# Performance work log

Measured on AMD Instinct MI355X. Metric: run time of the kernel, lower is better.

The kernel has to match this reference:

```python
import jax, jax.numpy as jnp
import numpy as np
import math

SEQ_LEN, PRED_LEN, CHANNELS, RANK = 720, 336, 862, 32
IN_LEN = SEQ_LEN // 2  # Haar low-pass with stride 2 (seq_len even)
BATCH = 256


def _dct2_ortho_mat(N):
    # D[k, n] = s_k * 2 * cos(pi * k * (2n+1) / (2N)); orthonormal DCT-II
    k = np.arange(N)[:, None]
    n = np.arange(N)[None, :]
    D = 2.0 * np.cos(np.pi * k * (2 * n + 1) / (2 * N))
    s = np.full(N, np.sqrt(1.0 / (2 * N)))
    s[0] = np.sqrt(1.0 / (4 * N))
    return jnp.asarray((s[:, None] * D).astype(np.float32))


def _idct2_unnorm_mat(N):
    # scipy.fft.idct(type=2, norm=None): out[n] = (1/N) * (x0/2 + sum_{k>=1} x_k cos(pi k (2n+1)/(2N)))
    # Returned as M[k, n] so that out = x @ M along last axis.
    k = np.arange(N)[:, None]
    n = np.arange(N)[None, :]
    M = np.cos(np.pi * k * (2 * n + 1) / (2 * N)) / N
    M[0, :] *= 0.5
    return jnp.asarray(M.astype(np.float32))


D_DCT = _dct2_ortho_mat(IN_LEN)        # [IN_LEN, IN_LEN]
M_IDCT = _idct2_unnorm_mat(PRED_LEN)   # [PRED_LEN, PRED_LEN]
INV_SQRT2 = 1.0 / math.sqrt(2.0)


def setup_inputs() -> dict:
    key = jax.random.key(0)
    k1, k2, k3, k4 = jax.random.split(key, 4)
    x = jax.random.normal(k1, (BATCH, SEQ_LEN, CHANNELS), dtype=jnp.float32)
    # kaiming_uniform-like scales for LowRank params
    boundA = math.sqrt(6.0 / IN_LEN)
    boundB = math.sqrt(6.0 / RANK)
    A = jax.random.uniform(k2, (IN_LEN, RANK), dtype=jnp.float32, minval=-boundA, maxval=boundA)
    B = jax.random.uniform(k3, (RANK, PRED_LEN), dtype=jnp.float32, minval=-boundB, maxval=boundB)
    b = jax.random.uniform(k4, (PRED_LEN,), dtype=jnp.float32)
    return {"x": x, "A": A, "B": B, "b": b}


def reference(x, A, B, b):
    # x: [B, L, C] -> [B, C, L]
    xt = jnp.transpose(x, (0, 2, 1))
    seq_mean = jnp.mean(xt, axis=-1, keepdims=True)          # [B, C, 1]
    xc = xt - seq_mean
    # Haar low-pass: depthwise conv1d with [1,1]/sqrt(2), stride 2
    h = (xc[..., ::2] + xc[..., 1::2]) * INV_SQRT2           # [B, C, IN_LEN]
    # orthonormal DCT-II along last axis, then divide by length
    y = jnp.einsum('bcn,kn->bck', h, D_DCT) / IN_LEN         # [B, C, IN_LEN]
    # low-rank prediction head (shared across channels)
    z = (y @ A) @ B + b                                      # [B, C, PRED_LEN]
    # unnormalized inverse DCT-II (scipy idct type=2, norm=None)
    o = z @ M_IDCT                                           # [B, C, PRED_LEN]
    o = o + seq_mean
    return jnp.transpose(o, (0, 2, 1))                       # [B, PRED_LEN, C]
```

## Files before the change

### kernel.cpp

```cpp
#include <hip/hip_runtime.h>
#include <math.h>

#define SEQ_LEN   720
#define IN_LEN    360
#define PRED_LEN  336
#define CHANNELS  862
#define RANK      32
#define BATCH     256

typedef _Float16 h2 __attribute__((ext_vector_type(2)));

#define WS_WH    0
#define WS_VH    5760
#define WS_CV    11136

#define L_EX     0
#define L_W      29376
#define L_V      35136
#define L_CV     40512

__device__ __forceinline__ float fdot2w(h2 a, h2 b, float c) {
#if __has_builtin(__builtin_amdgcn_fdot2)
    return __builtin_amdgcn_fdot2(a, b, c, false);
#else
    return fmaf((float)a[0], (float)b[0], fmaf((float)a[1], (float)b[1], c));
#endif
}
__device__ __forceinline__ h2 pkrtz(float a, float b) {
    return __builtin_bit_cast(h2, __builtin_amdgcn_cvt_pkrtz(a, b));
}
#define BC(u)  __builtin_bit_cast(h2, (u))
#define BCU(v) __builtin_bit_cast(unsigned, (v))

__device__ __forceinline__ void ntstore2(float* p, float2 v) {
    __builtin_nontemporal_store(__builtin_bit_cast(unsigned long long, v),
                                (unsigned long long*)p);
}

__global__ __launch_bounds__(256) void k_prep(const float* __restrict__ A,
                                              const float* __restrict__ B,
                                              const float* __restrict__ bias,
                                              unsigned* __restrict__ Wh,
                                              unsigned* __restrict__ Vh,
                                              float* __restrict__ cvec) {
    __shared__ float sbuf[IN_LEN * RANK];
    __shared__ float sres[256];
    const int t = threadIdx.x;
    int blk = blockIdx.x;
    if (blk < 45) {
        for (int i = t; i < IN_LEN * RANK; i += 256) sbuf[i] = A[i];
        __syncthreads();
        int n = blk * 8 + (t >> 5), r = t & 31;
        int step = 2 * n + 1, m = 0;
        float sum = 0.f;
        for (int k = 0; k < IN_LEN; ++k) {
            float coef = (k == 0) ? 0.05270462766947299f
                                  : 0.07453559924999299f;
            float d = coef * cospif((float)m * (1.0f / 720.0f));
            sum = fmaf(d, sbuf[k * RANK + r], sum);
            m += step; if (m >= 1440) m -= 1440;
        }
        sres[t] = sum * 0.0019641855032960957f;
        __syncthreads();
        if (t < 128) {
            int nl = t >> 4, j = t & 15;
            h2 v = pkrtz(sres[nl * 32 + 2 * j], sres[nl * 32 + 2 * j + 1]);
            Wh[(blk * 8 + nl) * 16 + j] = BCU(v);
        }
    } else if (blk < 87) {
        for (int i = t; i < PRED_LEN * RANK; i += 256) {
            int r = i / PRED_LEN, k = i - r * PRED_LEN;
            sbuf[k * RANK + r] = B[i];
        }
        __syncthreads();
        int n = (blk - 45) * 8 + (t >> 5), r = t & 31;
        int step = 2 * n + 1, m = 0;
        float sum = 0.f;
        for (int k = 0; k < PRED_LEN; ++k) {
            float mk = cospif((float)m * (1.0f / 672.0f));
            if (k == 0) mk *= 0.5f;
            sum = fmaf(mk, sbuf[k * RANK + r], sum);
            m += step; if (m >= 1344) m -= 1344;
        }
        sres[t] = sum * (1.0f / 336.0f);
        __syncthreads();
        if (t < 128) {
            int nl = t >> 4, j = t & 15;
            h2 v = pkrtz(sres[nl * 32 + 2 * j], sres[nl * 32 + 2 * j + 1]);
            Vh[((blk - 45) * 8 + nl) * 16 + j] = BCU(v);
        }
    } else {
        int n = (blk - 87) * 256 + t;
        if (n < PRED_LEN) {
            int step = 2 * n + 1, m = 0;
            float sum = 0.f;
            for (int k = 0; k < PRED_LEN; ++k) {
                float mk = cospif((float)m * (1.0f / 672.0f));
                if (k == 0) mk *= 0.5f;
                sum = fmaf(mk, bias[k], sum);
                m += step; if (m >= 1344) m -= 1344;
            }
            cvec[n] = sum * (1.0f / 336.0f);
        }
    }
}

__global__ __launch_bounds__(512) void k_main(const float* __restrict__ x,
                                              const float* __restrict__ A,
                                              const unsigned* __restrict__ Wh,
                                              const unsigned* __restrict__ Vh,
                                              const float* __restrict__ cvec,
                                              float* __restrict__ out) {
    __shared__ unsigned ldsu[40848];
    const int tid = threadIdx.x;
    const int b = blockIdx.x;
    const int h = tid >> 8;
    const int i = tid & 255;
    const bool active = (i < 216);
    const int c0 = (i < 215) ? 4 * i : 858;

    for (int idx = tid; idx < 1440; idx += 512)
        ((uint4*)(ldsu + L_W))[idx] = ((const uint4*)Wh)[idx];
    for (int idx = tid; idx < 1344; idx += 512)
        ((uint4*)(ldsu + L_V))[idx] = ((const uint4*)Vh)[idx];
    for (int idx = tid; idx < 84; idx += 512)
        ((uint4*)(ldsu + L_CV))[idx] = ((const uint4*)cvec)[idx];
    __syncthreads();

    h2 acc0[16], acc1[16], acc2[16], acc3[16];
    #pragma unroll
    for (int j = 0; j < 16; ++j) {
        acc0[j] = pkrtz(0.f, 0.f); acc1[j] = pkrtz(0.f, 0.f);
        acc2[j] = pkrtz(0.f, 0.f); acc3[j] = pkrtz(0.f, 0.f);
    }
    float S0 = 0.f, S1 = 0.f, S2 = 0.f, S3 = 0.f;

    if (active) {
        const float* xp = x + (size_t)b * (SEQ_LEN * CHANNELS)
                            + (size_t)h * (IN_LEN * CHANNELS) + c0;
        float2 b0[4], b1[4], b2[4], b3[4];
        #define LOADN(BUF, NL) { const float* p_ = xp + (size_t)(2 * (NL)) * CHANNELS; \
            BUF[0] = *(const float2*)(p_);                 \
            BUF[1] = *(const float2*)(p_ + 2);             \
            BUF[2] = *(const float2*)(p_ + CHANNELS);      \
            BUF[3] = *(const float2*)(p_ + CHANNELS + 2); }

        #define BODY(BUF, NL) { \
            float p0 = BUF[0].x + BUF[2].x; \
            float p1 = BUF[0].y + BUF[2].y; \
            float p2 = BUF[1].x + BUF[3].x; \
            float p3 = BUF[1].y + BUF[3].y; \
            S0 += p0; S1 += p1; S2 += p2; S3 += p3; \
            h2 P0 = pkrtz(p0, p0), P1 = pkrtz(p1, p1); \
            h2 P2 = pkrtz(p2, p2), P3 = pkrtz(p3, p3); \
            const uint4* wr = (const uint4*)(ldsu + L_W) + ((NL) + 180 * h) * 4; \
            _Pragma("unroll") \
            for (int q_ = 0; q_ < 4; ++q_) { \
                uint4 wv = wr[q_]; \
                h2 w0 = BC(wv.x), w1 = BC(wv.y), w2 = BC(wv.z), w3 = BC(wv.w); \
                acc0[4*q_+0] = w0 * P0 + acc0[4*q_+0]; \
                acc1[4*q_+0] = w0 * P1 + acc1[4*q_+0]; \
                acc2[4*q_+0] = w0 * P2 + acc2[4*q_+0]; \
                acc3[4*q_+0] = w0 * P3 + acc3[4*q_+0]; \
                acc0[4*q_+1] = w1 * P0 + acc0[4*q_+1]; \
                acc1[4*q_+1] = w1 * P1 + acc1[4*q_+1]; \
                acc2[4*q_+1] = w1 * P2 + acc2[4*q_+1]; \
                acc3[4*q_+1] = w1 * P3 + acc3[4*q_+1]; \
                acc0[4*q_+2] = w2 * P0 + acc0[4*q_+2]; \
                acc1[4*q_+2] = w2 * P1 + acc1[4*q_+2]; \
                acc2[4*q_+2] = w2 * P2 + acc2[4*q_+2]; \
                acc3[4*q_+2] = w2 * P3 + acc3[4*q_+2]; \
                acc0[4*q_+3] = w3 * P0 + acc0[4*q_+3]; \
                acc1[4*q_+3] = w3 * P1 + acc1[4*q_+3]; \
                acc2[4*q_+3] = w3 * P2 + acc2[4*q_+3]; \
                acc3[4*q_+3] = w3 * P3 + acc3[4*q_+3]; \
            } }

        LOADN(b0, 0) LOADN(b1, 1) LOADN(b2, 2)
        for (int it = 0; it < 45; ++it) {
            const int base = 4 * it;
            LOADN(b3, base + 3)
            BODY(b0, base)
            { int nn = (base + 4 < 180) ? base + 4 : 179; LOADN(b0, nn) }
            BODY(b1, base + 1)
            { int nn = (base + 5 < 180) ? base + 5 : 179; LOADN(b1, nn) }
            BODY(b2, base + 2)
            { int nn = (base + 6 < 180) ? base + 6 : 179; LOADN(b2, nn) }
            BODY(b3, base + 3)
        }
        #undef BODY
        #undef LOADN
    }

    if (active) {
        uint4* rec = (uint4*)(ldsu + (i + 216 * h) * 68);
        #pragma unroll
        for (int q = 0; q < 4; ++q) {
            uint4 v;
            v.x = BCU(acc0[4*q+0]); v.y = BCU(acc0[4*q+1]);
            v.z = BCU(acc0[4*q+2]); v.w = BCU(acc0[4*q+3]);
            rec[q] = v;
            v.x = BCU(acc1[4*q+0]); v.y = BCU(acc1[4*q+1]);
            v.z = BCU(acc1[4*q+2]); v.w = BCU(acc1[4*q+3]);
            rec[4 + q] = v;
            v.x = BCU(acc2[4*q+0]); v.y = BCU(acc2[4*q+1]);
            v.z = BCU(acc2[4*q+2]); v.w = BCU(acc2[4*q+3]);
            rec[8 + q] = v;
            v.x = BCU(acc3[4*q+0]); v.y = BCU(acc3[4*q+1]);
            v.z = BCU(acc3[4*q+2]); v.w = BCU(acc3[4*q+3]);
            rec[12 + q] = v;
        }
        uint4 sv;
        sv.x = __float_as_uint(S0); sv.y = __float_as_uint(S1);
        sv.z = __float_as_uint(S2); sv.w = __float_as_uint(S3);
        rec[16] = sv;
    }
    __syncthreads();

    if (active) {
        const uint4* pr = (const uint4*)(ldsu + (i + 216 * (1 - h)) * 68);
        #pragma unroll
        for (int q = 0; q < 4; ++q) {
            uint4 v = pr[q];
            acc0[4*q+0] = acc0[4*q+0] + BC(v.x); acc0[4*q+1] = acc0[4*q+1] + BC(v.y);
            acc0[4*q+2] = acc0[4*q+2] + BC(v.z); acc0[4*q+3] = acc0[4*q+3] + BC(v.w);
            v = pr[4 + q];
            acc1[4*q+0] = acc1[4*q+0] + BC(v.x); acc1[4*q+1] = acc1[4*q+1] + BC(v.y);
            acc1[4*q+2] = acc1[4*q+2] + BC(v.z); acc1[4*q+3] = acc1[4*q+3] + BC(v.w);
            v = pr[8 + q];
            acc2[4*q+0] = acc2[4*q+0] + BC(v.x); acc2[4*q+1] = acc2[4*q+1] + BC(v.y);
            acc2[4*q+2] = acc2[4*q+2] + BC(v.z); acc2[4*q+3] = acc2[4*q+3] + BC(v.w);
            v = pr[12 + q];
            acc3[4*q+0] = acc3[4*q+0] + BC(v.x); acc3[4*q+1] = acc3[4*q+1] + BC(v.y);
            acc3[4*q+2] = acc3[4*q+2] + BC(v.z); acc3[4*q+3] = acc3[4*q+3] + BC(v.w);
        }
        uint4 sv = pr[16];
        float S0f = S0 + __uint_as_float(sv.x), S1f = S1 + __uint_as_float(sv.y);
        float S2f = S2 + __uint_as_float(sv.z), S3f = S3 + __uint_as_float(sv.w);

        const float kc = (1.0f / 360.0f) * 0.037267799624996496f;
        float g0 = -S0f * kc, g1 = -S1f * kc, g2 = -S2f * kc, g3 = -S3f * kc;
        h2 G0 = pkrtz(g0, g0), G1 = pkrtz(g1, g1), G2 = pkrtz(g2, g2), G3 = pkrtz(g3, g3);
        #pragma unroll
        for (int q = 0; q < 8; ++q) {
            float4 a4 = ((const float4*)A)[q];
            h2 aa = pkrtz(a4.x, a4.y), ab = pkrtz(a4.z, a4.w);
            acc0[2*q]   = aa * G0 + acc0[2*q];   acc0[2*q+1] = ab * G0 + acc0[2*q+1];
            acc1[2*q]   = aa * G1 + acc1[2*q];   acc1[2*q+1] = ab * G1 + acc1[2*q+1];
            acc2[2*q]   = aa * G2 + acc2[2*q];   acc2[2*q+1] = ab * G2 + acc2[2*q+1];
            acc3[2*q]   = aa * G3 + acc3[2*q];   acc3[2*q+1] = ab * G3 + acc3[2*q+1];
        }
        const float mean0 = S0f * (1.0f / 720.0f), mean1 = S1f * (1.0f / 720.0f);
        const float mean2 = S2f * (1.0f / 720.0f), mean3 = S3f * (1.0f / 720.0f);

        float* op = out + (size_t)b * (PRED_LEN * CHANNELS)
                        + (size_t)(168 * h) * CHANNELS + c0;
        for (int nl = 0; nl < 168; ++nl) {
            const int n = 168 * h + nl;
            const uint4* vr = (const uint4*)(ldsu + L_V) + n * 4;
            float o0 = 0.f, o1 = 0.f, o2 = 0.f, o3 = 0.f;
            float e0 = 0.f, e1 = 0.f, e2 = 0.f, e3 = 0.f;
            #pragma unroll
            for (int q = 0; q < 4; ++q) {
                uint4 v = vr[q];
                h2 v0 = BC(v.x), v1 = BC(v.y), v2 = BC(v.z), v3 = BC(v.w);
                o0 = fdot2w(acc0[4*q+0], v0, o0); e0 = fdot2w(acc0[4*q+1], v1, e0);
                o1 = fdot2w(acc1[4*q+0], v0, o1); e1 = fdot2w(acc1[4*q+1], v1, e1);
                o2 = fdot2w(acc2[4*q+0], v0, o2); e2 = fdot2w(acc2[4*q+1], v1, e2);
                o3 = fdot2w(acc3[4*q+0], v0, o3); e3 = fdot2w(acc3[4*q+1], v1, e3);
                o0 = fdot2w(acc0[4*q+2], v2, o0); e0 = fdot2w(acc0[4*q+3], v3, e0);
                o1 = fdot2w(acc1[4*q+2], v2, o1); e1 = fdot2w(acc1[4*q+3], v3, e1);
                o2 = fdot2w(acc2[4*q+2], v2, o2); e2 = fdot2w(acc2[4*q+3], v3, e2);
                o3 = fdot2w(acc3[4*q+2], v2, o3); e3 = fdot2w(acc3[4*q+3], v3, e3);
            }
            float cvn = ((const float*)(ldsu + L_CV))[n];
            float2 w0, w1;
            w0.x = (o0 + e0) + cvn + mean0;
            w0.y = (o1 + e1) + cvn + mean1;
            w1.x = (o2 + e2) + cvn + mean2;
            w1.y = (o3 + e3) + cvn + mean3;
            ntstore2(op,     w0);
            ntstore2(op + 2, w1);
            op += CHANNELS;
        }
    }
}


extern "C" void kernel_launch(void* const* d_in, const int* in_sizes, int n_in,
                              void* d_out, int out_size, void* d_ws, size_t ws_size,
                              hipStream_t stream) {
    (void)in_sizes; (void)n_in; (void)out_size; (void)ws_size;
    const float* x    = (const float*)d_in[0];
    const float* A    = (const float*)d_in[1];
    const float* B    = (const float*)d_in[2];
    const float* bias = (const float*)d_in[3];
    float* out = (float*)d_out;

    unsigned* Wh   = (unsigned*)d_ws + WS_WH;
    unsigned* Vh   = (unsigned*)d_ws + WS_VH;
    float*    cvec = (float*)d_ws + WS_CV;

    k_prep<<<dim3(89), dim3(256), 0, stream>>>(A, B, bias, Wh, Vh, cvec);
    k_main<<<dim3(BATCH), dim3(512), 0, stream>>>(x, A, Wh, Vh, cvec, out);
}
```

Baseline: 249.0 us.

## Split channels across two blocks per batch and shrink LDS footprint

The grid becomes 2 x BATCH with 256-thread blocks, each block covering half the channels, where before one 512-thread block handled a whole batch. LDS is cut from about 160KB to about 59KB: the W matrix and the V matrix now share one region, with V loaded after the first phase. The cross-half accumulator exchange is done in two smaller rounds to fit the smaller buffer. The goal is more resident blocks per CU and better latency hiding, at the cost of extra barriers and reloading V from global memory after the reduction phase.

```diff
diff --git a/kernel.cpp b/kernel.cpp
--- a/kernel.cpp
+++ b/kernel.cpp
@@ -14,10 +14,10 @@
 #define WS_VH    5760
 #define WS_CV    11136
 
-#define L_EX     0
-#define L_W      29376
-#define L_V      35136
-#define L_CV     40512
+#define L_A      0
+#define L_EX     5760
+#define L_CV     14400
+#define L_TOT    14736
 
 __device__ __forceinline__ float fdot2w(h2 a, h2 b, float c) {
 #if __has_builtin(__builtin_amdgcn_fdot2)
@@ -32,7 +32,8 @@
 #define BC(u)  __builtin_bit_cast(h2, (u))
 #define BCU(v) __builtin_bit_cast(unsigned, (v))
 
-__device__ __forceinline__ void ntstore2(float* p, float2 v) {
+__device__ __forceinline__ void ntstore8(float* p, float a, float b) {
+    float2 v; v.x = a; v.y = b;
     __builtin_nontemporal_store(__builtin_bit_cast(unsigned long long, v),
                                 (unsigned long long*)p);
 }
@@ -105,25 +106,25 @@
     }
 }
 
-__global__ __launch_bounds__(512) void k_main(const float* __restrict__ x,
+__global__ __launch_bounds__(256) void k_main(const float* __restrict__ x,
                                               const float* __restrict__ A,
                                               const unsigned* __restrict__ Wh,
                                               const unsigned* __restrict__ Vh,
                                               const float* __restrict__ cvec,
                                               float* __restrict__ out) {
-    __shared__ unsigned ldsu[40848];
+    __shared__ unsigned ldsu[L_TOT];
     const int tid = threadIdx.x;
-    const int b = blockIdx.x;
-    const int h = tid >> 8;
-    const int i = tid & 255;
-    const bool active = (i < 216);
-    const int c0 = (i < 215) ? 4 * i : 858;
-
-    for (int idx = tid; idx < 1440; idx += 512)
-        ((uint4*)(ldsu + L_W))[idx] = ((const uint4*)Wh)[idx];
-    for (int idx = tid; idx < 1344; idx += 512)
-        ((uint4*)(ldsu + L_V))[idx] = ((const uint4*)Vh)[idx];
-    for (int idx = tid; idx < 84; idx += 512)
+    const int s = blockIdx.x;
+    const int b = blockIdx.y;
+    const int h = tid >> 7;
+    const int i = tid & 127;
+    const bool active = (i < 108);
+    int c0 = s * 432 + 4 * i;
+    if (c0 > 858) c0 = 858;
+
+    for (int idx = tid; idx < 1440; idx += 256)
+        ((uint4*)(ldsu + L_A))[idx] = ((const uint4*)Wh)[idx];
+    for (int idx = tid; idx < 84; idx += 256)
         ((uint4*)(ldsu + L_CV))[idx] = ((const uint4*)cvec)[idx];
     __syncthreads();
 
@@ -153,7 +154,7 @@
             S0 += p0; S1 += p1; S2 += p2; S3 += p3; \
             h2 P0 = pkrtz(p0, p0), P1 = pkrtz(p1, p1); \
             h2 P2 = pkrtz(p2, p2), P3 = pkrtz(p3, p3); \
-            const uint4* wr = (const uint4*)(ldsu + L_W) + ((NL) + 180 * h) * 4; \
+            const uint4* wr = (const uint4*)(ldsu + L_A) + ((NL) + 180 * h) * 4; \
             _Pragma("unroll") \
             for (int q_ = 0; q_ < 4; ++q_) { \
                 uint4 wv = wr[q_]; \
@@ -176,70 +177,87 @@
                 acc3[4*q_+3] = w3 * P3 + acc3[4*q_+3]; \
             } }
 
+        #define CL(nn) ((nn) < 180 ? (nn) : 179)
         LOADN(b0, 0) LOADN(b1, 1) LOADN(b2, 2)
         for (int it = 0; it < 45; ++it) {
             const int base = 4 * it;
-            LOADN(b3, base + 3)
-            BODY(b0, base)
-            { int nn = (base + 4 < 180) ? base + 4 : 179; LOADN(b0, nn) }
-            BODY(b1, base + 1)
-            { int nn = (base + 5 < 180) ? base + 5 : 179; LOADN(b1, nn) }
-            BODY(b2, base + 2)
-            { int nn = (base + 6 < 180) ? base + 6 : 179; LOADN(b2, nn) }
-            BODY(b3, base + 3)
-        }
+            LOADN(b3, base + 3)      BODY(b0, base)
+            LOADN(b0, CL(base + 4))  BODY(b1, base + 1)
+            LOADN(b1, CL(base + 5))  BODY(b2, base + 2)
+            LOADN(b2, CL(base + 6))  BODY(b3, base + 3)
+        }
+        #undef CL
         #undef BODY
         #undef LOADN
     }
-
-    if (active) {
-        uint4* rec = (uint4*)(ldsu + (i + 216 * h) * 68);
+    __syncthreads();
+
+    for (int idx = tid; idx < 1344; idx += 256)
+        ((uint4*)(ldsu + L_A))[idx] = ((const uint4*)Vh)[idx];
+    if (active) {
+        unsigned* rec = ldsu + L_EX + (i + 108 * h) * 40;
         #pragma unroll
         for (int q = 0; q < 4; ++q) {
             uint4 v;
             v.x = BCU(acc0[4*q+0]); v.y = BCU(acc0[4*q+1]);
             v.z = BCU(acc0[4*q+2]); v.w = BCU(acc0[4*q+3]);
-            rec[q] = v;
+            ((uint4*)rec)[q] = v;
             v.x = BCU(acc1[4*q+0]); v.y = BCU(acc1[4*q+1]);
             v.z = BCU(acc1[4*q+2]); v.w = BCU(acc1[4*q+3]);
-            rec[4 + q] = v;
+            ((uint4*)rec)[4 + q] = v;
+        }
+        rec[32] = __float_as_uint(S0);
+        rec[33] = __float_as_uint(S1);
+    }
+    __syncthreads();
+    if (active) {
+        const unsigned* pr = ldsu + L_EX + (i + 108 * (1 - h)) * 40;
+        #pragma unroll
+        for (int q = 0; q < 4; ++q) {
+            uint4 v = ((const uint4*)pr)[q];
+            acc0[4*q+0] = acc0[4*q+0] + BC(v.x); acc0[4*q+1] = acc0[4*q+1] + BC(v.y);
+            acc0[4*q+2] = acc0[4*q+2] + BC(v.z); acc0[4*q+3] = acc0[4*q+3] + BC(v.w);
+            v = ((const uint4*)pr)[4 + q];
+            acc1[4*q+0] = acc1[4*q+0] + BC(v.x); acc1[4*q+1] = acc1[4*q+1] + BC(v.y);
+            acc1[4*q+2] = acc1[4*q+2] + BC(v.z); acc1[4*q+3] = acc1[4*q+3] + BC(v.w);
+        }
+        S0 += __uint_as_float(pr[32]);
+        S1 += __uint_as_float(pr[33]);
+    }
+    __syncthreads();
+
+    if (active) {
+        unsigned* rec = ldsu + L_EX + (i + 108 * h) * 40;
+        #pragma unroll
+        for (int q = 0; q < 4; ++q) {
+            uint4 v;
             v.x = BCU(acc2[4*q+0]); v.y = BCU(acc2[4*q+1]);
             v.z = BCU(acc2[4*q+2]); v.w = BCU(acc2[4*q+3]);
-            rec[8 + q] = v;
+            ((uint4*)rec)[q] = v;
             v.x = BCU(acc3[4*q+0]); v.y = BCU(acc3[4*q+1]);
             v.z = BCU(acc3[4*q+2]); v.w = BCU(acc3[4*q+3]);
-            rec[12 + q] = v;
-        }
-        uint4 sv;
-        sv.x = __float_as_uint(S0); sv.y = __float_as_uint(S1);
-        sv.z = __float_as_uint(S2); sv.w = __float_as_uint(S3);
-        rec[16] = sv;
-    }
-    __syncthreads();
-
-    if (active) {
-        const uint4* pr = (const uint4*)(ldsu + (i + 216 * (1 - h)) * 68);
+            ((uint4*)rec)[4 + q] = v;
+        }
+        rec[32] = __float_as_uint(S2);
+        rec[33] = __float_as_uint(S3);
+    }
+    __syncthreads();
+    if (active) {
+        const unsigned* pr = ldsu + L_EX + (i + 108 * (1 - h)) * 40;
         #pragma unroll
         for (int q = 0; q < 4; ++q) {
-            uint4 v = pr[q];
-            acc0[4*q+0] = acc0[4*q+0] + BC(v.x); acc0[4*q+1] = acc0[4*q+1] + BC(v.y);
-            acc0[4*q+2] = acc0[4*q+2] + BC(v.z); acc0[4*q+3] = acc0[4*q+3] + BC(v.w);
-            v = pr[4 + q];
-            acc1[4*q+0] = acc1[4*q+0] + BC(v.x); acc1[4*q+1] = acc1[4*q+1] + BC(v.y);
-            acc1[4*q+2] = acc1[4*q+2] + BC(v.z); acc1[4*q+3] = acc1[4*q+3] + BC(v.w);
-            v = pr[8 + q];
+            uint4 v = ((const uint4*)pr)[q];
             acc2[4*q+0] = acc2[4*q+0] + BC(v.x); acc2[4*q+1] = acc2[4*q+1] + BC(v.y);
             acc2[4*q+2] = acc2[4*q+2] + BC(v.z); acc2[4*q+3] = acc2[4*q+3] + BC(v.w);
-            v = pr[12 + q];
+            v = ((const uint4*)pr)[4 + q];
             acc3[4*q+0] = acc3[4*q+0] + BC(v.x); acc3[4*q+1] = acc3[4*q+1] + BC(v.y);
             acc3[4*q+2] = acc3[4*q+2] + BC(v.z); acc3[4*q+3] = acc3[4*q+3] + BC(v.w);
         }
-        uint4 sv = pr[16];
-        float S0f = S0 + __uint_as_float(sv.x), S1f = S1 + __uint_as_float(sv.y);
-        float S2f = S2 + __uint_as_float(sv.z), S3f = S3 + __uint_as_float(sv.w);
+        S2 += __uint_as_float(pr[32]);
+        S3 += __uint_as_float(pr[33]);
 
         const float kc = (1.0f / 360.0f) * 0.037267799624996496f;
-        float g0 = -S0f * kc, g1 = -S1f * kc, g2 = -S2f * kc, g3 = -S3f * kc;
+        float g0 = -S0 * kc, g1 = -S1 * kc, g2 = -S2 * kc, g3 = -S3 * kc;
         h2 G0 = pkrtz(g0, g0), G1 = pkrtz(g1, g1), G2 = pkrtz(g2, g2), G3 = pkrtz(g3, g3);
         #pragma unroll
         for (int q = 0; q < 8; ++q) {
@@ -250,14 +268,14 @@
             acc2[2*q]   = aa * G2 + acc2[2*q];   acc2[2*q+1] = ab * G2 + acc2[2*q+1];
             acc3[2*q]   = aa * G3 + acc3[2*q];   acc3[2*q+1] = ab * G3 + acc3[2*q+1];
         }
-        const float mean0 = S0f * (1.0f / 720.0f), mean1 = S1f * (1.0f / 720.0f);
-        const float mean2 = S2f * (1.0f / 720.0f), mean3 = S3f * (1.0f / 720.0f);
+        const float mean0 = S0 * (1.0f / 720.0f), mean1 = S1 * (1.0f / 720.0f);
+        const float mean2 = S2 * (1.0f / 720.0f), mean3 = S3 * (1.0f / 720.0f);
 
         float* op = out + (size_t)b * (PRED_LEN * CHANNELS)
                         + (size_t)(168 * h) * CHANNELS + c0;
         for (int nl = 0; nl < 168; ++nl) {
             const int n = 168 * h + nl;
-            const uint4* vr = (const uint4*)(ldsu + L_V) + n * 4;
+            const uint4* vr = (const uint4*)(ldsu + L_A) + n * 4;
             float o0 = 0.f, o1 = 0.f, o2 = 0.f, o3 = 0.f;
             float e0 = 0.f, e1 = 0.f, e2 = 0.f, e3 = 0.f;
             #pragma unroll
@@ -274,13 +292,8 @@
                 o3 = fdot2w(acc3[4*q+2], v2, o3); e3 = fdot2w(acc3[4*q+3], v3, e3);
             }
             float cvn = ((const float*)(ldsu + L_CV))[n];
-            float2 w0, w1;
-            w0.x = (o0 + e0) + cvn + mean0;
-            w0.y = (o1 + e1) + cvn + mean1;
-            w1.x = (o2 + e2) + cvn + mean2;
-            w1.y = (o3 + e3) + cvn + mean3;
-            ntstore2(op,     w0);
-            ntstore2(op + 2, w1);
+            ntstore8(op,     (o0 + e0) + cvn + mean0, (o1 + e1) + cvn + mean1);
+            ntstore8(op + 2, (o2 + e2) + cvn + mean2, (o3 + e3) + cvn + mean3);
             op += CHANNELS;
         }
     }
@@ -302,5 +315,5 @@
     float*    cvec = (float*)d_ws + WS_CV;
 
     k_prep<<<dim3(89), dim3(256), 0, stream>>>(A, B, bias, Wh, Vh, cvec);
-    k_main<<<dim3(BATCH), dim3(512), 0, stream>>>(x, A, Wh, Vh, cvec, out);
-}
+    k_main<<<dim3(2, BATCH), dim3(256), 0, stream>>>(x, A, Wh, Vh, cvec, out);
+}
```

Result: slower. 275.3 us (+10.5%).
